# Optimization experiments

Hardware: AMD Instinct MI355X
Metric: run time of the kernel (lower is better)

The kernel has to match this reference:

```python
import jax, jax.numpy as jnp
import numpy as np

B, S, D, H, DFF = 8, 1024, 1024, 16, 4096
DK = D // H
EPS = 1e-6
NEG = -1e9


def setup_inputs() -> dict:
    key = jax.random.key(0)
    ks = jax.random.split(key, 8)
    x = jax.random.normal(ks[0], (B, S, D), dtype=jnp.float32)
    mask = jnp.ones((B, 1, 1, S), dtype=jnp.int32)
    s = 0.02
    wq = jax.random.normal(ks[1], (D, D), jnp.float32) * s
    wk = jax.random.normal(ks[2], (D, D), jnp.float32) * s
    wv = jax.random.normal(ks[3], (D, D), jnp.float32) * s
    wo = jax.random.normal(ks[4], (D, D), jnp.float32) * s
    bq = jnp.zeros((D,), jnp.float32); bk = jnp.zeros((D,), jnp.float32)
    bv = jnp.zeros((D,), jnp.float32); bo = jnp.zeros((D,), jnp.float32)
    w1 = jax.random.normal(ks[5], (D, DFF), jnp.float32) * s
    b1 = jnp.zeros((DFF,), jnp.float32)
    w2 = jax.random.normal(ks[6], (DFF, D), jnp.float32) * s
    b2 = jnp.zeros((D,), jnp.float32)
    g1 = jnp.array(1.0, jnp.float32); be1 = jnp.array(0.0, jnp.float32)
    g2 = jnp.array(1.0, jnp.float32); be2 = jnp.array(0.0, jnp.float32)
    return dict(x=x, mask=mask, wq=wq, bq=bq, wk=wk, bk=bk, wv=wv, bv=bv,
                wo=wo, bo=bo, w1=w1, b1=b1, w2=w2, b2=b2,
                g1=g1, be1=be1, g2=g2, be2=be2)


def layer_norm(x, gamma, beta):
    # repo quirk: unbiased std (ddof=1), scalar gamma/beta, divide by (std+eps)
    mean = jnp.mean(x, axis=-1, keepdims=True)
    std = jnp.std(x, axis=-1, keepdims=True, ddof=1)
    return gamma * (x - mean) / (std + EPS) + beta


def mha(x, mask, wq, bq, wk, bk, wv, bv, wo, bo):
    q = (x @ wq + bq).reshape(B, S, H, DK).transpose(0, 2, 1, 3)  # bhsd
    k = (x @ wk + bk).reshape(B, S, H, DK).transpose(0, 2, 1, 3)
    v = (x @ wv + bv).reshape(B, S, H, DK).transpose(0, 2, 1, 3)
    scores = jnp.einsum('bhqd,bhkd->bhqk', q, k) / jnp.sqrt(jnp.float32(DK))
    scores = jnp.where(mask == 0, NEG, scores)
    attn = jax.nn.softmax(scores, axis=-1)
    out = jnp.einsum('bhqk,bhkd->bhqd', attn, v)
    out = out.transpose(0, 2, 1, 3).reshape(B, S, D)
    return out @ wo + bo


def reference(x, mask, wq, bq, wk, bk, wv, bv, wo, bo, w1, b1, w2, b2, g1, be1, g2, be2):
    # pre-LN residual: x + sublayer(norm(x)); dropout inert at eval
    x = x + mha(layer_norm(x, g1, be1), mask, wq, bq, wk, bk, wv, bv, wo, bo)
    h = layer_norm(x, g2, be2)
    x = x + (jax.nn.relu(h @ w1 + b1) @ w2 + b2)
    return x
```

## Files before the change

### kernel.cpp

```cpp
#include <hip/hip_runtime.h>
#include <math.h>

typedef __bf16 bf16;
typedef float f32x4 __attribute__((ext_vector_type(4)));
typedef float f32x16 __attribute__((ext_vector_type(16)));
typedef bf16 bf16x8 __attribute__((ext_vector_type(8)));
typedef bf16 bf16x4 __attribute__((ext_vector_type(4)));
typedef unsigned int u32;
typedef unsigned int u32x2 __attribute__((ext_vector_type(2)));

#define DEV __device__ __forceinline__

constexpr int Ss = 1024, Dd = 1024;
constexpr float EPSf = 1e-6f;
constexpr float SM_SCALE = 0.125f * 1.4426950408889634f;

DEV void gl_lds16(const void* g, void* l) {
  __builtin_amdgcn_global_load_lds(
      (const __attribute__((address_space(1))) void*)g,
      (__attribute__((address_space(3))) void*)l, 16, 0, 0);
}

DEV u32 cvtpk(float lo, float hi) {
  u32 r;
  asm("v_cvt_pk_bf16_f32 %0, %1, %2" : "=v"(r) : "v"(lo), "v"(hi));
  return r;
}

__global__ __launch_bounds__(256) void transpose6_k(
    const float* __restrict__ i0, const float* __restrict__ i1,
    const float* __restrict__ i2, const float* __restrict__ i3,
    const float* __restrict__ i4, const float* __restrict__ i5,
    bf16* __restrict__ o0, bf16* __restrict__ o1, bf16* __restrict__ o2,
    bf16* __restrict__ o3, bf16* __restrict__ o4, bf16* __restrict__ o5) {
  __shared__ float t[64 * 65];
  const int bi = blockIdx.x;
  const float* in;
  bf16* out;
  int R, C, local, sh;
  if (bi < 1024) {
    const int j = bi >> 8;
    local = bi & 255; R = 1024; C = 1024; sh = 4;
    in = (j == 0) ? i0 : (j == 1) ? i1 : (j == 2) ? i2 : i3;
    out = (j == 0) ? o0 : (j == 1) ? o1 : (j == 2) ? o2 : o3;
  } else if (bi < 2048) {
    local = bi - 1024; R = 1024; C = 4096; sh = 6; in = i4; out = o4;
  } else {
    local = bi - 2048; R = 4096; C = 1024; sh = 4; in = i5; out = o5;
  }
  const int nx = 1 << sh;
  const int bx = local & (nx - 1), by = local >> sh;
  const int tid = threadIdx.x;
  const int tx = tid & 63, ty = tid >> 6;
  const int r0 = by * 64, c0 = bx * 64;
#pragma unroll
  for (int i = 0; i < 16; i++) {
    int r = ty + i * 4;
    t[r * 65 + tx] = in[(size_t)(r0 + r) * C + c0 + tx];
  }
  __syncthreads();
#pragma unroll
  for (int i = 0; i < 16; i++) {
    int r = ty + i * 4;
    out[(size_t)(c0 + r) * R + r0 + tx] = (bf16)t[tx * 65 + r];
  }
}

__global__ __launch_bounds__(256) void ln_kernel(
    const float* __restrict__ in, bf16* __restrict__ out,
    const float* __restrict__ gp, const float* __restrict__ bp) {
  const int row = blockIdx.x;
  const int tid = threadIdx.x;
  float v[4];
  const float* p = in + (size_t)row * Dd + tid * 4;
#pragma unroll
  for (int i = 0; i < 4; i++) v[i] = p[i];
  float s = v[0] + v[1] + v[2] + v[3];
  float s2 = v[0] * v[0] + v[1] * v[1] + v[2] * v[2] + v[3] * v[3];
#pragma unroll
  for (int m = 1; m < 64; m <<= 1) {
    s += __shfl_xor(s, m, 64);
    s2 += __shfl_xor(s2, m, 64);
  }
  __shared__ float ls[4], ls2[4];
  if ((tid & 63) == 0) {
    ls[tid >> 6] = s;
    ls2[tid >> 6] = s2;
  }
  __syncthreads();
  s = ls[0] + ls[1] + ls[2] + ls[3];
  s2 = ls2[0] + ls2[1] + ls2[2] + ls2[3];
  float mean = s * (1.0f / Dd);
  float var = (s2 - (float)Dd * mean * mean) * (1.0f / (Dd - 1));
  var = fmaxf(var, 0.0f);
  float g = gp[0], be = bp[0];
  float rs = g / (sqrtf(var) + EPSf);
  bf16* q = out + (size_t)row * Dd + tid * 4;
#pragma unroll
  for (int i = 0; i < 4; i++) q[i] = (bf16)((v[i] - mean) * rs + be);
}

template <int EPI, int BK>
__global__ __launch_bounds__(256) void gemm_bt(
    const bf16* __restrict__ A, const bf16* __restrict__ Bt,
    const float* __restrict__ bias, const float* __restrict__ bias2,
    const float* __restrict__ bias3, const float* __restrict__ resid,
    bf16* __restrict__ vtb, void* __restrict__ Cout, int M, int N, int K,
    int sa, int sb) {
  __shared__ __attribute__((aligned(16))) char smem[2 * 128 * BK * 2];
  bf16* As = (bf16*)smem;
  bf16* Bs = (bf16*)(smem + 128 * BK * 2);
  constexpr int CPR = BK / 8;
  constexpr int RPJ = 256 / CPR;
  constexpr int NJ = BK / 16;
  const int tid = threadIdx.x;
  const int ln = tid & 63;
  const int wv = tid >> 6;
  const int wm = wv >> 1, wn = wv & 1;
  const int quad = ln >> 4, l16 = ln & 15;
  const int l7 = l16 & 7;
  const int nxg = gridDim.x;
  const int d = blockIdx.y * nxg + blockIdx.x;
  const int sseq = d >> 3;
  const int bxr = sseq % nxg;
  const int byr = (d & 7) + 8 * (sseq / nxg);
  const int m0 = byr * 128, n0 = bxr * 128;

  f32x4 acc[4][4];
#pragma unroll
  for (int i = 0; i < 4; i++)
#pragma unroll
    for (int j = 0; j < 4; j++) acc[i][j] = {0.f, 0.f, 0.f, 0.f};

  const int sr = tid / CPR;
  const int sc = (tid & (CPR - 1)) ^ (sr & 7);
  const size_t abase = (size_t)(m0 + sr) * sa + sc * 8;
  const size_t bbase = (size_t)(n0 + sr) * sb + sc * 8;

  for (int k0 = 0; k0 < K; k0 += BK) {
#pragma unroll
    for (int j = 0; j < NJ; j++) {
      gl_lds16(A + abase + (size_t)(j * RPJ) * sa + k0,
               (char*)As + j * 4096 + wv * 1024);
      gl_lds16(Bt + bbase + (size_t)(j * RPJ) * sb + k0,
               (char*)Bs + j * 4096 + wv * 1024);
    }
    __syncthreads();
#pragma unroll
    for (int kh = 0; kh < BK / 32; kh++) {
      bf16x8 af[4], bfr[4];
#pragma unroll
      for (int mi = 0; mi < 4; mi++)
        af[mi] = *(const bf16x8*)&As[(wm * 64 + mi * 16 + l16) * BK +
                                     ((kh * 4 + quad) ^ l7) * 8];
#pragma unroll
      for (int ni = 0; ni < 4; ni++)
        bfr[ni] = *(const bf16x8*)&Bs[(wn * 64 + ni * 16 + l16) * BK +
                                      ((kh * 4 + quad) ^ l7) * 8];
#pragma unroll
      for (int mi = 0; mi < 4; mi++)
#pragma unroll
        for (int ni = 0; ni < 4; ni++)
          acc[mi][ni] = __builtin_amdgcn_mfma_f32_16x16x32_bf16(
              af[mi], bfr[ni], acc[mi][ni], 0, 0, 0);
    }
    __syncthreads();
  }

  if constexpr (EPI == 4) {
    if (n0 < 2048) {
#pragma unroll
      for (int mi = 0; mi < 4; mi++) {
        const int m = m0 + wm * 64 + mi * 16 + quad * 4;
#pragma unroll
        for (int ni = 0; ni < 4; ni++) {
          const int n = n0 + wn * 64 + ni * 16 + l16;
          const float bvl = (n < 1024) ? bias[n] : bias2[n - 1024];
#pragma unroll
          for (int r = 0; r < 4; r++)
            ((bf16*)Cout)[(size_t)(m + r) * N + n] =
                (bf16)(acc[mi][ni][r] + bvl);
        }
      }
    } else {
      bf16* T = (bf16*)smem;
#pragma unroll
      for (int mi = 0; mi < 4; mi++) {
        const int ml = wm * 64 + mi * 16 + quad * 4;
        const int c = ml >> 3, hf = (ml >> 2) & 1;
#pragma unroll
        for (int ni = 0; ni < 4; ni++) {
          const int nl = wn * 64 + ni * 16 + l16;
          const float bvl = bias3[(n0 - 2048) + nl];
          bf16x4 tv;
#pragma unroll
          for (int r = 0; r < 4; r++) tv[r] = (bf16)(acc[mi][ni][r] + bvl);
          *(bf16x4*)&T[nl * 128 + ((c ^ (nl & 15)) << 3) + (hf << 2)] = tv;
        }
      }
      __syncthreads();
      const size_t vbase =
          ((size_t)(m0 >> 10) * 1024 + (n0 - 2048)) * Ss + (m0 & 1023);
#pragma unroll
      for (int p = 0; p < 8; p++) {
        const int row = p * 16 + (tid >> 4);
        const int k = tid & 15;
        bf16x8 vv = *(const bf16x8*)&T[row * 128 + ((k ^ (row & 15)) << 3)];
        *(bf16x8*)&vtb[vbase + (size_t)row * Ss + k * 8] = vv;
      }
    }
  } else {
#pragma unroll
    for (int mi = 0; mi < 4; mi++) {
      const int m = m0 + wm * 64 + mi * 16 + quad * 4;
#pragma unroll
      for (int ni = 0; ni < 4; ni++) {
        const int n = n0 + wn * 64 + ni * 16 + l16;
        float bvl = 0.0f;
        if constexpr (EPI != 3) bvl = bias[n];
#pragma unroll
        for (int r = 0; r < 4; r++) {
          float val = acc[mi][ni][r] + bvl;
          const size_t idx = (size_t)(m + r) * N + n;
          if constexpr (EPI == 1) {
            ((float*)Cout)[idx] = val + resid[idx];
          } else if constexpr (EPI == 2) {
            ((bf16*)Cout)[idx] = (bf16)fmaxf(val, 0.0f);
          } else {
            ((float*)Cout)[idx] = val + resid[idx];
          }
        }
      }
    }
  }
}

__global__ __launch_bounds__(256) void attn_k(
    const bf16* __restrict__ qkv, const bf16* __restrict__ vt,
    const int* __restrict__ mask, bf16* __restrict__ ctx) {
  __shared__ __attribute__((aligned(16))) char smem[36864];
  __shared__ int Ft[16];
  bf16* Qs = (bf16*)smem;
  bf16* Ks = (bf16*)(smem + 16384);
  bf16* Vs = (bf16*)(smem + 24576);
  float* Fm = (float*)(smem + 32768);
  const int tid = threadIdx.x;
  const int l = tid & 63, w = tid >> 6;
  const int lq = l & 31, lh = l >> 5;
  const int lq7 = lq & 7;
  const int bh = blockIdx.x;
  const int b = bh >> 4, h = bh & 15;
  const int q0 = blockIdx.y * 128;
  const int sr = tid >> 3;
  const int sc = (tid & 7) ^ (sr & 7);

  if (tid < 16) Ft[tid] = 0;
  {
#pragma unroll
    for (int j = 0; j < 4; j++) {
      const size_t ga =
          (size_t)(b * Ss + q0 + j * 32 + sr) * 3072 + h * 64 + sc * 8;
      gl_lds16(qkv + ga, (char*)Qs + j * 4096 + w * 1024);
    }
  }
  __syncthreads();

  bf16x8 qf[4];
#pragma unroll
  for (int s = 0; s < 4; s++)
    qf[s] =
        *(const bf16x8*)&Qs[(w * 32 + lq) * 64 + (((s * 2 + lh) ^ lq7) * 8)];

  {
    const int4 mv = *(const int4*)&mask[b * Ss + tid * 4];
    const float ninf = -__builtin_inff();
    Fm[tid * 4 + 0] = mv.x ? 0.0f : ninf;
    Fm[tid * 4 + 1] = mv.y ? 0.0f : ninf;
    Fm[tid * 4 + 2] = mv.z ? 0.0f : ninf;
    Fm[tid * 4 + 3] = mv.w ? 0.0f : ninf;
    if (!(mv.x && mv.y && mv.z && mv.w)) atomicOr(&Ft[tid >> 4], 1);
  }

  f32x16 oacc[2];
#pragma unroll
  for (int d = 0; d < 2; d++)
#pragma unroll
    for (int r = 0; r < 16; r++) oacc[d][r] = 0.0f;
  float rsum = 0.0f;

  for (int kk0 = 0; kk0 < Ss; kk0 += 64) {
    {
#pragma unroll
      for (int j = 0; j < 2; j++) {
        const size_t ga = (size_t)(b * Ss + kk0 + j * 32 + sr) * 3072 + 1024 +
                          h * 64 + sc * 8;
        gl_lds16(qkv + ga, (char*)Ks + j * 4096 + w * 1024);
        const size_t gv = (size_t)(bh * 64 + j * 32 + sr) * Ss + kk0 + sc * 8;
        gl_lds16(vt + gv, (char*)Vs + j * 4096 + w * 1024);
      }
    }
    __syncthreads();

    f32x16 sacc[2];
#pragma unroll
    for (int kb = 0; kb < 2; kb++)
#pragma unroll
      for (int r = 0; r < 16; r++) sacc[kb][r] = 0.0f;

    __builtin_amdgcn_s_setprio(1);
#pragma unroll
    for (int kb = 0; kb < 2; kb++)
#pragma unroll
      for (int s = 0; s < 4; s++) {
        const bf16x8 kf = *(const bf16x8*)&Ks[(kb * 32 + lq) * 64 +
                                              (((s * 2 + lh) ^ lq7) * 8)];
        sacc[kb] = __builtin_amdgcn_mfma_f32_32x32x16_bf16(kf, qf[s],
                                                           sacc[kb], 0, 0, 0);
      }
    __builtin_amdgcn_s_setprio(0);

    if (__builtin_amdgcn_readfirstlane(Ft[kk0 >> 6])) {
#pragma unroll
      for (int kb = 0; kb < 2; kb++)
#pragma unroll
        for (int g = 0; g < 4; g++) {
          const f32x4 mv = *(const f32x4*)&Fm[kk0 + kb * 32 + 4 * lh + 8 * g];
#pragma unroll
          for (int j = 0; j < 4; j++)
            sacc[kb][g * 4 + j] = __builtin_amdgcn_exp2f(
                fmaf(sacc[kb][g * 4 + j], SM_SCALE, mv[j]));
        }
    } else {
#pragma unroll
      for (int kb = 0; kb < 2; kb++)
#pragma unroll
        for (int r = 0; r < 16; r++)
          sacc[kb][r] = __builtin_amdgcn_exp2f(sacc[kb][r] * SM_SCALE);
    }
#pragma unroll
    for (int kb = 0; kb < 2; kb++) {
      const float t0 = (sacc[kb][0] + sacc[kb][1]) + (sacc[kb][2] + sacc[kb][3]);
      const float t1 = (sacc[kb][4] + sacc[kb][5]) + (sacc[kb][6] + sacc[kb][7]);
      const float t2 =
          (sacc[kb][8] + sacc[kb][9]) + (sacc[kb][10] + sacc[kb][11]);
      const float t3 =
          (sacc[kb][12] + sacc[kb][13]) + (sacc[kb][14] + sacc[kb][15]);
      rsum += ((t0 + t1) + (t2 + t3));
    }

    __builtin_amdgcn_s_setprio(1);
#pragma unroll
    for (int t = 0; t < 4; t++) {
      const int kb = t >> 1, rb = (t & 1) * 8;
      u32 pa = cvtpk(sacc[kb][rb + 0], sacc[kb][rb + 1]);
      u32 pbv = cvtpk(sacc[kb][rb + 2], sacc[kb][rb + 3]);
      u32 pc = cvtpk(sacc[kb][rb + 4], sacc[kb][rb + 5]);
      u32 pd = cvtpk(sacc[kb][rb + 6], sacc[kb][rb + 7]);
      asm("v_permlane32_swap_b32 %0, %1" : "+v"(pa), "+v"(pc));
      asm("v_permlane32_swap_b32 %0, %1" : "+v"(pbv), "+v"(pd));
      union {
        u32 u[4];
        bf16x8 v;
      } pk;
      pk.u[0] = pa;
      pk.u[1] = pbv;
      pk.u[2] = pc;
      pk.u[3] = pd;
      const int vsw = ((t * 2 + lh) ^ lq7) * 8;
      const bf16x8 vf0 = *(const bf16x8*)&Vs[lq * 64 + vsw];
      const bf16x8 vf1 = *(const bf16x8*)&Vs[(32 + lq) * 64 + vsw];
      oacc[0] =
          __builtin_amdgcn_mfma_f32_32x32x16_bf16(vf0, pk.v, oacc[0], 0, 0, 0);
      oacc[1] =
          __builtin_amdgcn_mfma_f32_32x32x16_bf16(vf1, pk.v, oacc[1], 0, 0, 0);
    }
    __builtin_amdgcn_s_setprio(0);
    __syncthreads();
  }

  float xs = rsum, ys = rsum;
  asm("v_permlane32_swap_b32 %0, %1" : "+v"(xs), "+v"(ys));
  const float inv = 1.0f / (xs + ys);

  bf16* Tb = (bf16*)(smem + w * 4608);
#pragma unroll
  for (int dblk = 0; dblk < 2; dblk++)
#pragma unroll
    for (int g = 0; g < 4; g++) {
      const u32 lo =
          cvtpk(oacc[dblk][g * 4 + 0] * inv, oacc[dblk][g * 4 + 1] * inv);
      const u32 hi =
          cvtpk(oacc[dblk][g * 4 + 2] * inv, oacc[dblk][g * 4 + 3] * inv);
      u32x2 pr2;
      pr2[0] = lo;
      pr2[1] = hi;
      const int dbase = dblk * 32 + 8 * g + 4 * lh;
      *(u32x2*)&Tb[lq * 72 + dbase] = pr2;
    }
  __syncthreads();
#pragma unroll
  for (int p = 0; p < 4; p++) {
    const int row = p * 8 + (l >> 3);
    const int ch = l & 7;
    const bf16x8 vv = *(const bf16x8*)&Tb[row * 72 + ch * 8];
    *(bf16x8*)&ctx[(size_t)(b * Ss + q0 + w * 32 + row) * Dd + h * 64 +
                   ch * 8] = vv;
  }
}

extern "C" void kernel_launch(void* const* d_in, const int* in_sizes, int n_in,
                              void* d_out, int out_size, void* d_ws,
                              size_t ws_size, hipStream_t stream) {
  (void)in_sizes; (void)n_in; (void)out_size;
  const float* x = (const float*)d_in[0];
  const int* mask = (const int*)d_in[1];
  const float* wq = (const float*)d_in[2];
  const float* bq = (const float*)d_in[3];
  const float* wk = (const float*)d_in[4];
  const float* bk = (const float*)d_in[5];
  const float* wvw = (const float*)d_in[6];
  const float* bv = (const float*)d_in[7];
  const float* wo = (const float*)d_in[8];
  const float* bo = (const float*)d_in[9];
  const float* w1 = (const float*)d_in[10];
  const float* b1 = (const float*)d_in[11];
  const float* w2 = (const float*)d_in[12];
  const float* b2 = (const float*)d_in[13];
  const float* g1 = (const float*)d_in[14];
  const float* be1 = (const float*)d_in[15];
  const float* g2 = (const float*)d_in[16];
  const float* be2 = (const float*)d_in[17];
  float* out = (float*)d_out;

  char* ws = (char*)d_ws;
  const size_t MB = 1024 * 1024;
  bf16* w1T = (bf16*)(ws + 0 * MB);
  bf16* w2T = (bf16*)(ws + 8 * MB);
  bf16* wqkvT = (bf16*)(ws + 16 * MB);
  bf16* woT = (bf16*)(ws + 22 * MB);
  bf16* lnb = (bf16*)(ws + 24 * MB);
  bf16* qkv = (bf16*)(ws + 40 * MB);
  bf16* vtb = (bf16*)(ws + 88 * MB);
  float* x1 = (float*)(ws + 40 * MB);
  bf16* ctx = lnb;

  dim3 blk(256);
  transpose6_k<<<3072, blk, 0, stream>>>(
      wq, wk, wvw, wo, w1, w2, wqkvT, wqkvT + (size_t)1024 * 1024,
      wqkvT + (size_t)2048 * 1024, woT, w1T, w2T);
  ln_kernel<<<8192, blk, 0, stream>>>(x, lnb, g1, be1);
  gemm_bt<4, 64><<<dim3(24, 64), blk, 0, stream>>>(
      lnb, wqkvT, bq, bk, bv, nullptr, vtb, qkv, 8192, 3072, 1024, 1024, 1024);
  attn_k<<<dim3(128, 8), blk, 0, stream>>>(qkv, vtb, mask, ctx);
  gemm_bt<1, 128><<<dim3(8, 64), blk, 0, stream>>>(
      ctx, woT, bo, nullptr, nullptr, x, nullptr, x1, 8192, 1024, 1024, 1024,
      1024);
  ln_kernel<<<8192, blk, 0, stream>>>(x1, lnb, g2, be2);

  if (ws_size >= 136 * MB) {
    bf16* mid = (bf16*)(ws + 72 * MB);
    gemm_bt<2, 64><<<dim3(32, 64), blk, 0, stream>>>(
        lnb, w1T, b1, nullptr, nullptr, nullptr, nullptr, mid, 8192, 4096,
        1024, 1024, 1024);
    gemm_bt<1, 128><<<dim3(8, 64), blk, 0, stream>>>(
        mid, w2T, b2, nullptr, nullptr, x1, nullptr, out, 8192, 1024, 4096,
        4096, 4096);
  } else {
    bf16* mid = (bf16*)(ws + 72 * MB);
    gemm_bt<2, 64><<<dim3(16, 64), blk, 0, stream>>>(
        lnb, w1T, b1, nullptr, nullptr, nullptr, nullptr, mid, 8192, 2048,
        1024, 1024, 1024);
    gemm_bt<1, 128><<<dim3(8, 64), blk, 0, stream>>>(
        mid, w2T, b2, nullptr, nullptr, x1, nullptr, out, 8192, 1024, 2048,
        2048, 4096);
    gemm_bt<2, 64><<<dim3(16, 64), blk, 0, stream>>>(
        lnb, w1T + (size_t)2048 * 1024, b1 + 2048, nullptr, nullptr, nullptr,
        nullptr, mid, 8192, 2048, 1024, 1024, 1024);
    gemm_bt<3, 128><<<dim3(8, 64), blk, 0, stream>>>(
        mid, w2T + 2048, nullptr, nullptr, nullptr, out, nullptr, out, 8192,
        1024, 2048, 2048, 4096);
  }
}
```

Baseline: 462.2 us.

## Add 256x256-tile 512-thread GEMM with ReLU epilogue for FFN up-projection

Adds a dedicated GEMM kernel for the first FFN matmul. It uses 256x256 output tiles, 8 waves, double-buffered 128KB LDS filled by direct global-to-LDS loads, a grouped block swizzle for L2 locality, and s_setprio around the MFMA bursts. The larger tile raises arithmetic intensity and cuts redundant A/B reloads compared with the generic 64-wide tile kernel. In exchange, the 128KB shared footprint and large accumulator set allow only one block per CU, and the grid becomes coarser (512 blocks), which may leave the tail less balanced.

```diff
diff --git a/kernel.cpp b/kernel.cpp
--- a/kernel.cpp
+++ b/kernel.cpp
@@ -235,6 +235,115 @@
   }
 }
 
+__global__ __launch_bounds__(512) void gemm256_relu(
+    const bf16* __restrict__ A, const bf16* __restrict__ Bt,
+    const float* __restrict__ bias, bf16* __restrict__ Cout, int M, int N,
+    int K, int sa, int sb) {
+  __shared__ __attribute__((aligned(16))) char smem[131072];
+  const int tid = threadIdx.x;
+  const int ln = tid & 63;
+  const int wv = tid >> 6;
+  const int wm = wv >> 2, wn = wv & 3;
+  const int quad = ln >> 4, l16 = ln & 15;
+  const int l7 = l16 & 7;
+  const int nxg = gridDim.x;
+  const int d = blockIdx.y * nxg + blockIdx.x;
+  const int sseq = d >> 3;
+  const int bxr = sseq % nxg;
+  const int byr = (d & 7) + 8 * (sseq / nxg);
+  const int m0 = byr * 256, n0 = bxr * 256;
+
+  f32x4 acc[8][4];
+#pragma unroll
+  for (int i = 0; i < 8; i++)
+#pragma unroll
+    for (int j = 0; j < 4; j++) acc[i][j] = {0.f, 0.f, 0.f, 0.f};
+
+  const int sr = tid >> 3;
+  const int sc = (tid & 7) ^ (sr & 7);
+  const size_t abase = (size_t)(m0 + sr) * sa + sc * 8;
+  const size_t bbase = (size_t)(n0 + sr) * sb + sc * 8;
+  const int w8 = tid >> 6;
+
+  const int nt = K >> 6;
+  int cur = 0;
+
+  {
+#pragma unroll
+    for (int j = 0; j < 4; j++) {
+      gl_lds16(A + abase + (size_t)(j * 64) * sa,
+               smem + j * 8192 + w8 * 1024);
+      gl_lds16(Bt + bbase + (size_t)(j * 64) * sb,
+               smem + 32768 + j * 8192 + w8 * 1024);
+    }
+  }
+
+  for (int t = 0; t < nt; ++t) {
+    if (t + 1 < nt) {
+      char* ldst = smem + (cur ^ 1) * 65536;
+      const int koff = (t + 1) * 64;
+#pragma unroll
+      for (int j = 0; j < 4; j++) {
+        gl_lds16(A + abase + (size_t)(j * 64) * sa + koff,
+                 ldst + j * 8192 + w8 * 1024);
+        gl_lds16(Bt + bbase + (size_t)(j * 64) * sb + koff,
+                 ldst + 32768 + j * 8192 + w8 * 1024);
+      }
+      asm volatile("s_waitcnt vmcnt(8)" ::: "memory");
+    } else {
+      asm volatile("s_waitcnt vmcnt(0)" ::: "memory");
+    }
+    __builtin_amdgcn_s_barrier();
+
+    const bf16* As = (const bf16*)(smem + cur * 65536);
+    const bf16* Bs = (const bf16*)(smem + cur * 65536 + 32768);
+    bf16x8 bfr[4][2];
+#pragma unroll
+    for (int ni = 0; ni < 4; ni++)
+#pragma unroll
+      for (int kh = 0; kh < 2; kh++)
+        bfr[ni][kh] = *(const bf16x8*)&Bs[(wn * 64 + ni * 16 + l16) * 64 +
+                                          (((kh * 4 + quad) ^ l7) * 8)];
+#pragma unroll
+    for (int p = 0; p < 4; p++) {
+      bf16x8 af[2][2];
+#pragma unroll
+      for (int m2 = 0; m2 < 2; m2++)
+#pragma unroll
+        for (int kh = 0; kh < 2; kh++)
+          af[m2][kh] =
+              *(const bf16x8*)&As[(wm * 128 + (p * 2 + m2) * 16 + l16) * 64 +
+                                  (((kh * 4 + quad) ^ l7) * 8)];
+      __builtin_amdgcn_s_setprio(1);
+#pragma unroll
+      for (int m2 = 0; m2 < 2; m2++)
+#pragma unroll
+        for (int ni = 0; ni < 4; ni++)
+#pragma unroll
+          for (int kh = 0; kh < 2; kh++)
+            acc[p * 2 + m2][ni] = __builtin_amdgcn_mfma_f32_16x16x32_bf16(
+                af[m2][kh], bfr[ni][kh], acc[p * 2 + m2][ni], 0, 0, 0);
+      __builtin_amdgcn_s_setprio(0);
+    }
+    __builtin_amdgcn_s_barrier();
+    cur ^= 1;
+  }
+
+#pragma unroll
+  for (int mi = 0; mi < 8; mi++) {
+    const int m = m0 + wm * 128 + mi * 16 + quad * 4;
+#pragma unroll
+    for (int ni = 0; ni < 4; ni++) {
+      const int n = n0 + wn * 64 + ni * 16 + l16;
+      const float bvl = bias[n];
+#pragma unroll
+      for (int r = 0; r < 4; r++)
+        Cout[(size_t)(m + r) * N + n] =
+            (bf16)fmaxf(acc[mi][ni][r] + bvl, 0.0f);
+    }
+  }
+}
+
 __global__ __launch_bounds__(256) void attn_k(
     const bf16* __restrict__ qkv, const bf16* __restrict__ vt,
     const int* __restrict__ mask, bf16* __restrict__ ctx) {
@@ -459,23 +568,21 @@
 
   if (ws_size >= 136 * MB) {
     bf16* mid = (bf16*)(ws + 72 * MB);
-    gemm_bt<2, 64><<<dim3(32, 64), blk, 0, stream>>>(
-        lnb, w1T, b1, nullptr, nullptr, nullptr, nullptr, mid, 8192, 4096,
-        1024, 1024, 1024);
+    gemm256_relu<<<dim3(16, 32), dim3(512), 0, stream>>>(
+        lnb, w1T, b1, mid, 8192, 4096, 1024, 1024, 1024);
     gemm_bt<1, 128><<<dim3(8, 64), blk, 0, stream>>>(
         mid, w2T, b2, nullptr, nullptr, x1, nullptr, out, 8192, 1024, 4096,
         4096, 4096);
   } else {
     bf16* mid = (bf16*)(ws + 72 * MB);
-    gemm_bt<2, 64><<<dim3(16, 64), blk, 0, stream>>>(
-        lnb, w1T, b1, nullptr, nullptr, nullptr, nullptr, mid, 8192, 2048,
-        1024, 1024, 1024);
+    gemm256_relu<<<dim3(8, 32), dim3(512), 0, stream>>>(
+        lnb, w1T, b1, mid, 8192, 2048, 1024, 1024, 1024);
     gemm_bt<1, 128><<<dim3(8, 64), blk, 0, stream>>>(
         mid, w2T, b2, nullptr, nullptr, x1, nullptr, out, 8192, 1024, 2048,
         2048, 4096);
-    gemm_bt<2, 64><<<dim3(16, 64), blk, 0, stream>>>(
-        lnb, w1T + (size_t)2048 * 1024, b1 + 2048, nullptr, nullptr, nullptr,
-        nullptr, mid, 8192, 2048, 1024, 1024, 1024);
+    gemm256_relu<<<dim3(8, 32), dim3(512), 0, stream>>>(
+        lnb, w1T + (size_t)2048 * 1024, b1 + 2048, mid, 8192, 2048, 1024,
+        1024, 1024);
     gemm_bt<3, 128><<<dim3(8, 64), blk, 0, stream>>>(
         mid, w2T + 2048, nullptr, nullptr, nullptr, out, nullptr, out, 8192,
         1024, 2048, 2048, 4096);
```

Result: faster. 442.9 us (-4.2%).
